# Performance work log

Measured on AMD Instinct MI355X. Metric: run time of the kernel, lower is better.

Reference implementation:

```python
import jax, jax.numpy as jnp
import numpy as np
from jax import lax

B, QL, N_IN, H = 64, 2048, 256, 64


def setup_inputs() -> dict:
    key = jax.random.key(0)
    ks = jax.random.split(key, 8)
    s = 1.0 / np.sqrt(H)  # PyTorch LSTMCell init scale
    return {
        "h_concat": jax.random.normal(ks[0], (B, QL, N_IN), dtype=jnp.float32),
        "w21": jax.random.normal(ks[1], (N_IN, 1), dtype=jnp.float32),
        "w22": jax.random.normal(ks[2], (H, 1), dtype=jnp.float32),
        "bias2": jax.random.normal(ks[3], (1,), dtype=jnp.float32),
        "W_ih": jax.random.uniform(ks[4], (4 * H, N_IN + 1), dtype=jnp.float32, minval=-s, maxval=s),
        "W_hh": jax.random.uniform(ks[5], (4 * H, H), dtype=jnp.float32, minval=-s, maxval=s),
        "b_ih": jax.random.uniform(ks[6], (4 * H,), dtype=jnp.float32, minval=-s, maxval=s),
        "b_hh": jax.random.uniform(ks[7], (4 * H,), dtype=jnp.float32, minval=-s, maxval=s),
    }


def reference(h_concat, w21, w22, bias2, W_ih, W_hh, b_ih, b_hh):
    Bsz, T, n_in = h_concat.shape
    nh = W_hh.shape[1]

    def step(carry, x):
        h, c = carry  # [B,H] each; x: [B,n_in]
        # sigmoid gate: pz_t = sigmoid(x @ w21 + h @ w22 + bias2) -> [B,1]
        pz = jax.nn.sigmoid(x @ w21 + h @ w22 + bias2)
        hz = jnp.concatenate([x, pz], axis=1)  # [B, n_in+1]
        # LSTMCell (PyTorch gate order: i, f, g, o)
        gates = hz @ W_ih.T + b_ih + h @ W_hh.T + b_hh  # [B,4H]
        i, f, g, o = jnp.split(gates, 4, axis=1)
        c_new = jax.nn.sigmoid(f) * c + jax.nn.sigmoid(i) * jnp.tanh(g)
        h_new = jax.nn.sigmoid(o) * jnp.tanh(c_new)
        return (h_new, c_new), pz[:, 0]

    h0 = jnp.zeros((Bsz, nh), dtype=h_concat.dtype)
    c0 = jnp.zeros((Bsz, nh), dtype=h_concat.dtype)
    xs = jnp.swapaxes(h_concat, 0, 1)  # [T,B,n_in]
    _, Z = lax.scan(step, (h0, c0), xs)  # Z: [T,B]
    return jnp.swapaxes(Z, 0, 1)  # [B,T]
```

## Files before the change

kernel.cpp:

```cpp
#include <hip/hip_runtime.h>

#define TT 2048
#define BB 64

typedef _Float16 v2h __attribute__((ext_vector_type(2)));
typedef _Float16 v4h __attribute__((ext_vector_type(4)));
typedef float v4f __attribute__((ext_vector_type(4)));

__device__ __forceinline__ float frcp(float x) { return __builtin_amdgcn_rcpf(x); }
__device__ __forceinline__ float fsig(float x) { return frcp(1.f + __expf(-x)); }
__device__ __forceinline__ float ftan(float x) { return 1.f - 2.f * frcp(1.f + __expf(2.f * x)); }

#if __has_builtin(__builtin_amdgcn_fdot2)
#define FDOT2(a, b, c) __builtin_amdgcn_fdot2((a), (b), (c), false)
#else
#define FDOT2(a, b, c) ((c) + (float)(a).x * (float)(b).x + (float)(a).y * (float)(b).y)
#endif

#define DPPADD(x, ctrl)                                                        \
  (x) += __builtin_bit_cast(float, __builtin_amdgcn_update_dpp(                \
             0, __builtin_bit_cast(int, (x)), (ctrl), 0xf, 0xf, true))

__device__ __forceinline__ float wave_sum64(float x) {
  DPPADD(x, 0x111);
  DPPADD(x, 0x112);
  DPPADD(x, 0x114);
  DPPADD(x, 0x118);
  DPPADD(x, 0x142);
  DPPADD(x, 0x143);
  return __builtin_bit_cast(
      float, __builtin_amdgcn_readlane(__builtin_bit_cast(int, x), 63));
}

__global__ __launch_bounds__(256) void gates_gemm_mfma(
    const float* __restrict__ X, const float* __restrict__ W,
    const float* __restrict__ bih, const float* __restrict__ bhh,
    float* __restrict__ G, int t0, int Tc) {
  __shared__ __align__(16) _Float16 Xs[64][40];
  __shared__ __align__(16) _Float16 Ws[128][40];
  const int tid = threadIdx.x;
  const int m0 = blockIdx.x * 64;
  const int n0 = blockIdx.y * 128;
  const int bb = m0 / Tc;
  const int tt0 = m0 - bb * Tc;
  const int w = tid >> 6, l = tid & 63;
  const int lr = l & 15, lk = l >> 4;

  const int srow = tid >> 2, skq = (tid & 3) * 8;
  const int wri = tid >> 1, wkh = (tid & 1) * 16;
  const float* xrow = X + (size_t)(bb * TT + t0 + tt0 + srow) * 256 + skq;
  const float* wrow = W + (size_t)(n0 + wri) * 257 + wkh;

  float bsum[8];
#pragma unroll
  for (int nf = 0; nf < 8; ++nf)
    bsum[nf] = bih[n0 + nf * 16 + lr] + bhh[n0 + nf * 16 + lr];

  v4f acc[8];
#pragma unroll
  for (int nf = 0; nf < 8; ++nf) acc[nf] = (v4f){0.f, 0.f, 0.f, 0.f};

  for (int k0 = 0; k0 < 256; k0 += 32) {
    float xa[8], wa[16];
#pragma unroll
    for (int u = 0; u < 8; ++u) xa[u] = xrow[k0 + u];
#pragma unroll
    for (int u = 0; u < 16; ++u) wa[u] = wrow[k0 + u];
    if (k0 != 0) __syncthreads();
    {
      uint xw[4];
#pragma unroll
      for (int u = 0; u < 4; ++u) {
        v2h p; p.x = (_Float16)xa[2*u]; p.y = (_Float16)xa[2*u+1];
        xw[u] = __builtin_bit_cast(uint, p);
      }
      *reinterpret_cast<uint4*>(&Xs[srow][skq]) =
          make_uint4(xw[0], xw[1], xw[2], xw[3]);
      uint ww[8];
#pragma unroll
      for (int u = 0; u < 8; ++u) {
        v2h p; p.x = (_Float16)wa[2*u]; p.y = (_Float16)wa[2*u+1];
        ww[u] = __builtin_bit_cast(uint, p);
      }
      *reinterpret_cast<uint4*>(&Ws[wri][wkh]) =
          make_uint4(ww[0], ww[1], ww[2], ww[3]);
      *reinterpret_cast<uint4*>(&Ws[wri][wkh + 8]) =
          make_uint4(ww[4], ww[5], ww[6], ww[7]);
    }
    __syncthreads();
    const v4h a0 = *reinterpret_cast<const v4h*>(&Xs[w * 16 + lr][lk * 4]);
    const v4h a1 = *reinterpret_cast<const v4h*>(&Xs[w * 16 + lr][16 + lk * 4]);
#pragma unroll
    for (int nf = 0; nf < 8; ++nf) {
      const v4h b0 = *reinterpret_cast<const v4h*>(&Ws[nf * 16 + lr][lk * 4]);
      const v4h b1 = *reinterpret_cast<const v4h*>(&Ws[nf * 16 + lr][16 + lk * 4]);
      acc[nf] = __builtin_amdgcn_mfma_f32_16x16x16f16(a0, b0, acc[nf], 0, 0, 0);
      acc[nf] = __builtin_amdgcn_mfma_f32_16x16x16f16(a1, b1, acc[nf], 0, 0, 0);
    }
  }
  const int grow = m0 + w * 16 + lk * 4;
#pragma unroll
  for (int nf = 0; nf < 8; ++nf) {
#pragma unroll
    for (int j = 0; j < 4; ++j) {
      G[(size_t)(grow + j) * 256 + n0 + nf * 16 + lr] = acc[nf][j] + bsum[nf];
    }
  }
}

__global__ __launch_bounds__(256) void pz_kernel(const float* __restrict__ X,
                                                 const float* __restrict__ w21,
                                                 const float* __restrict__ bias2,
                                                 float* __restrict__ P,
                                                 int t0, int Tc) {
  const int r = blockIdx.x * 4 + (threadIdx.x >> 6);
  const int lane = threadIdx.x & 63;
  const int bb = r / Tc;
  const int tt = r - bb * Tc;
  const float4 xv = *reinterpret_cast<const float4*>(
      &X[((size_t)(bb * TT + t0 + tt)) * 256 + lane * 4]);
  const float4 wv = *reinterpret_cast<const float4*>(&w21[lane * 4]);
  float s = xv.x*wv.x + xv.y*wv.y + xv.z*wv.z + xv.w*wv.w;
#pragma unroll
  for (int o = 32; o; o >>= 1) s += __shfl_xor(s, o);
  if (lane == 0) P[r] = s + bias2[0];
}

__global__ __launch_bounds__(64, 1) void lstm_seq7(
    const float* __restrict__ G, const float* __restrict__ P,
    const float* __restrict__ Wih, const float* __restrict__ Whh,
    const float* __restrict__ w22, float* __restrict__ Z,
    float* __restrict__ hq, float* __restrict__ cq, int t0, int Tc) {
  const int l = threadIdx.x;
  const int b = blockIdx.x;
  __shared__ __align__(16) _Float16 hsm[64];

  v2h wh[4][32];
#pragma unroll
  for (int q = 0; q < 4; ++q) {
#pragma unroll
    for (int j = 0; j < 16; ++j) {
      float4 v = *reinterpret_cast<const float4*>(&Whh[(size_t)(q*64 + l)*64 + 4*j]);
      v2h pA, pB;
      pA.x = (_Float16)v.x; pA.y = (_Float16)v.y;
      pB.x = (_Float16)v.z; pB.y = (_Float16)v.w;
      wh[q][2*j] = pA; wh[q][2*j+1] = pB;
    }
  }
  float wihL[4];
#pragma unroll
  for (int q = 0; q < 4; ++q) wihL[q] = Wih[(size_t)(q*64 + l)*257 + 256];
  const float w22r = w22[l];

  float h = 0.f, c = 0.f;
  if (t0 != 0) { h = hq[b * 64 + l]; c = cq[b * 64 + l]; }
  hsm[l] = (_Float16)h;
  __builtin_amdgcn_wave_barrier();

  const float* Gb = G + (size_t)b * Tc * 256 + l;
  const float* Pb = P + (size_t)b * Tc;
  float* Zb = Z + (size_t)b * TT + t0;

  float gr[4][4], pr[4];
#pragma unroll
  for (int u = 0; u < 4; ++u) {
    const float* Gt = Gb + (size_t)u * 256;
#pragma unroll
    for (int q = 0; q < 4; ++q) gr[u][q] = Gt[q * 64];
    pr[u] = Pb[u];
  }

  for (int tt = 0; tt < Tc; tt += 4) {
    float zs[4];
#pragma unroll
    for (int uu = 0; uu < 4; ++uu) {
      const int step = tt + uu;
      const float gx0 = gr[uu][0], gx1 = gr[uu][1];
      const float gx2 = gr[uu][2], gx3 = gr[uu][3];
      const float p0 = pr[uu];
      int pf = step + 4; if (pf > Tc - 1) pf = Tc - 1;
      {
        const float* Gt = Gb + (size_t)pf * 256;
#pragma unroll
        for (int q = 0; q < 4; ++q) gr[uu][q] = Gt[q * 64];
        pr[uu] = Pb[pf];
      }

      const float tot = wave_sum64(h * w22r);
      const float pz = fsig(tot + p0);

      float d0a=0.f,d0b=0.f,d1a=0.f,d1b=0.f,d2a=0.f,d2b=0.f,d3a=0.f,d3b=0.f;
      const uint4* hp = reinterpret_cast<const uint4*>(hsm);
#pragma unroll
      for (int jj = 0; jj < 8; ++jj) {
        const uint4 uq = hp[jj];
        const v2h ha = __builtin_bit_cast(v2h, uq.x);
        const v2h hb = __builtin_bit_cast(v2h, uq.y);
        const v2h hc = __builtin_bit_cast(v2h, uq.z);
        const v2h hd = __builtin_bit_cast(v2h, uq.w);
        d0a = FDOT2(ha, wh[0][4*jj+0], d0a); d0b = FDOT2(hb, wh[0][4*jj+1], d0b);
        d0a = FDOT2(hc, wh[0][4*jj+2], d0a); d0b = FDOT2(hd, wh[0][4*jj+3], d0b);
        d1a = FDOT2(ha, wh[1][4*jj+0], d1a); d1b = FDOT2(hb, wh[1][4*jj+1], d1b);
        d1a = FDOT2(hc, wh[1][4*jj+2], d1a); d1b = FDOT2(hd, wh[1][4*jj+3], d1b);
        d2a = FDOT2(ha, wh[2][4*jj+0], d2a); d2b = FDOT2(hb, wh[2][4*jj+1], d2b);
        d2a = FDOT2(hc, wh[2][4*jj+2], d2a); d2b = FDOT2(hd, wh[2][4*jj+3], d2b);
        d3a = FDOT2(ha, wh[3][4*jj+0], d3a); d3b = FDOT2(hb, wh[3][4*jj+1], d3b);
        d3a = FDOT2(hc, wh[3][4*jj+2], d3a); d3b = FDOT2(hd, wh[3][4*jj+3], d3b);
      }
      const float pre0 = gx0 + pz * wihL[0] + (d0a + d0b);
      const float pre1 = gx1 + pz * wihL[1] + (d1a + d1b);
      const float pre2 = gx2 + pz * wihL[2] + (d2a + d2b);
      const float pre3 = gx3 + pz * wihL[3] + (d3a + d3b);

      const float ai = fsig(pre0);
      const float af = fsig(pre1);
      const float ag = ftan(pre2);
      const float ao = fsig(pre3);
      c = af * c + ai * ag;
      h = ao * ftan(c);

      __builtin_amdgcn_wave_barrier();
      hsm[l] = (_Float16)h;
      __builtin_amdgcn_wave_barrier();
      zs[uu] = pz;
    }
    if (l == 0) {
      float4 zo; zo.x = zs[0]; zo.y = zs[1]; zo.z = zs[2]; zo.w = zs[3];
      *reinterpret_cast<float4*>(&Zb[tt]) = zo;
    }
  }
  hq[b * 64 + l] = h;
  cq[b * 64 + l] = c;
}

__global__ __launch_bounds__(256) void lstm_fallback(const float* __restrict__ X,
    const float* __restrict__ w21, const float* __restrict__ w22,
    const float* __restrict__ bias2, const float* __restrict__ Wih,
    const float* __restrict__ Whh, const float* __restrict__ bih,
    const float* __restrict__ bhh, float* __restrict__ Z) {
  const int b = blockIdx.x;
  const int g = threadIdx.x;
  const int lane = g & 63;
  __shared__ __align__(16) float h_s[64];
  __shared__ float act_s[256];
  __shared__ __align__(16) float x_s[256];
  __shared__ __align__(16) float w21_s[256];
  float wh[64];
#pragma unroll
  for (int j = 0; j < 64; j += 4) {
    float4 v = *reinterpret_cast<const float4*>(&Whh[(size_t)g*64 + j]);
    wh[j]=v.x; wh[j+1]=v.y; wh[j+2]=v.z; wh[j+3]=v.w;
  }
  const float wihL = Wih[(size_t)g*257 + 256];
  const float bias = bih[g] + bhh[g];
  const float b2 = bias2[0];
  const float w22r = w22[lane];
  w21_s[g] = w21[g];
  if (g < 64) h_s[g] = 0.f;
  float c = 0.f;
  __syncthreads();
  const float* Wr = Wih + (size_t)g * 257;
  for (int t = 0; t < TT; ++t) {
    x_s[g] = X[((size_t)b*TT + t)*256 + g];
    __syncthreads();
    float pv = h_s[lane] * w22r;
    {
      const float4 xq = *reinterpret_cast<const float4*>(&x_s[lane*4]);
      const float4 wq = *reinterpret_cast<const float4*>(&w21_s[lane*4]);
      pv += xq.x*wq.x + xq.y*wq.y + xq.z*wq.z + xq.w*wq.w;
    }
#pragma unroll
    for (int o = 32; o; o >>= 1) pv += __shfl_xor(pv, o);
    const float pz = fsig(pv + b2);
    float a0=0.f, a1=0.f, a2=0.f, a3=0.f;
#pragma unroll
    for (int j = 0; j < 64; j += 4) {
      float4 hv = *reinterpret_cast<const float4*>(&h_s[j]);
      a0 += hv.x*wh[j]; a1 += hv.y*wh[j+1]; a2 += hv.z*wh[j+2]; a3 += hv.w*wh[j+3];
    }
    float xd0=0.f, xd1=0.f, xd2=0.f, xd3=0.f;
    for (int k = 0; k < 256; k += 4) {
      const float4 xq = *reinterpret_cast<const float4*>(&x_s[k]);
      xd0 += xq.x*Wr[k]; xd1 += xq.y*Wr[k+1]; xd2 += xq.z*Wr[k+2]; xd3 += xq.w*Wr[k+3];
    }
    const float pre = bias + pz*wihL + ((a0+a1)+(a2+a3)) + ((xd0+xd1)+(xd2+xd3));
    act_s[g] = ((g >> 6) == 2) ? ftan(pre) : fsig(pre);
    if (g == 0) Z[(size_t)b*TT + t] = pz;
    __syncthreads();
    if (g < 64) {
      const float iv = act_s[g], fv = act_s[64+g], gv = act_s[128+g], ov = act_s[192+g];
      c = fv*c + iv*gv;
      h_s[g] = ov * ftan(c);
    }
    __syncthreads();
  }
}

extern "C" void kernel_launch(void* const* d_in, const int* in_sizes, int n_in,
                              void* d_out, int out_size, void* d_ws, size_t ws_size,
                              hipStream_t stream) {
  const float* X     = (const float*)d_in[0];
  const float* w21   = (const float*)d_in[1];
  const float* w22   = (const float*)d_in[2];
  const float* bias2 = (const float*)d_in[3];
  const float* Wih   = (const float*)d_in[4];
  const float* Whh   = (const float*)d_in[5];
  const float* bih   = (const float*)d_in[6];
  const float* bhh   = (const float*)d_in[7];
  float* Z = (float*)d_out;

  int Tc = 0;
  for (int cand = 2048; cand >= 64; cand >>= 1) {
    size_t need = (size_t)cand * (64*256*4 + 64*4) + 2*64*64*4;
    if (ws_size >= need) { Tc = cand; break; }
  }
  if (Tc == 0) {
    lstm_fallback<<<dim3(64), dim3(256), 0, stream>>>(X, w21, w22, bias2, Wih, Whh, bih, bhh, Z);
    return;
  }
  float* Gbuf = (float*)d_ws;
  float* Pbuf = Gbuf + (size_t)64 * Tc * 256;
  float* hq   = Pbuf + (size_t)64 * Tc;
  float* cq   = hq + 64 * 64;
  for (int t0 = 0; t0 < 2048; t0 += Tc) {
    gates_gemm_mfma<<<dim3(Tc, 2), dim3(256), 0, stream>>>(X, Wih, bih, bhh,
                                                           Gbuf, t0, Tc);
    pz_kernel<<<dim3(16 * Tc), dim3(256), 0, stream>>>(X, w21, bias2, Pbuf, t0, Tc);
    lstm_seq7<<<dim3(BB), dim3(64), 0, stream>>>(
        Gbuf, Pbuf, Wih, Whh, w22, Z, hq, cq, t0, Tc);
  }
}
```

Baseline: 1.049 ms.

## Fuse pz projection into gates GEMM and widen recurrent dot-product accumulators

The separate pz_kernel is removed. The x·w21 projection is now computed inside the gates GEMM from the fp32 X values already loaded there, with w21 staged in shared memory and a 4-lane shuffle reduction. This saves one kernel launch and a second full read of X per chunk. The recurrent FDOT2 loop also uses four independent accumulators per gate instead of two, shortening the dependent chain on the serial LSTM critical path at the cost of more registers.

Measured after the change: 1.117 ms. 6.5% more time.

```diff
diff --git a/kernel.cpp b/kernel.cpp
--- a/kernel.cpp
+++ b/kernel.cpp
@@ -35,9 +35,11 @@
 __global__ __launch_bounds__(256) void gates_gemm_mfma(
     const float* __restrict__ X, const float* __restrict__ W,
     const float* __restrict__ bih, const float* __restrict__ bhh,
-    float* __restrict__ G, int t0, int Tc) {
+    const float* __restrict__ w21, const float* __restrict__ bias2,
+    float* __restrict__ G, float* __restrict__ P, int t0, int Tc) {
   __shared__ __align__(16) _Float16 Xs[64][40];
   __shared__ __align__(16) _Float16 Ws[128][40];
+  __shared__ float w21s[256];
   const int tid = threadIdx.x;
   const int m0 = blockIdx.x * 64;
   const int n0 = blockIdx.y * 128;
@@ -45,12 +47,15 @@
   const int tt0 = m0 - bb * Tc;
   const int w = tid >> 6, l = tid & 63;
   const int lr = l & 15, lk = l >> 4;
+  const bool do_pz = (blockIdx.y == 0);
 
   const int srow = tid >> 2, skq = (tid & 3) * 8;
   const int wri = tid >> 1, wkh = (tid & 1) * 16;
   const float* xrow = X + (size_t)(bb * TT + t0 + tt0 + srow) * 256 + skq;
   const float* wrow = W + (size_t)(n0 + wri) * 257 + wkh;
 
+  w21s[tid] = w21[tid];
+
   float bsum[8];
 #pragma unroll
   for (int nf = 0; nf < 8; ++nf)
@@ -59,6 +64,7 @@
   v4f acc[8];
 #pragma unroll
   for (int nf = 0; nf < 8; ++nf) acc[nf] = (v4f){0.f, 0.f, 0.f, 0.f};
+  float psum = 0.f;
 
   for (int k0 = 0; k0 < 256; k0 += 32) {
     float xa[8], wa[16];
@@ -88,6 +94,10 @@
           make_uint4(ww[4], ww[5], ww[6], ww[7]);
     }
     __syncthreads();
+    if (do_pz) {
+#pragma unroll
+      for (int u = 0; u < 8; ++u) psum += xa[u] * w21s[k0 + skq + u];
+    }
     const v4h a0 = *reinterpret_cast<const v4h*>(&Xs[w * 16 + lr][lk * 4]);
     const v4h a1 = *reinterpret_cast<const v4h*>(&Xs[w * 16 + lr][16 + lk * 4]);
 #pragma unroll
@@ -98,6 +108,11 @@
       acc[nf] = __builtin_amdgcn_mfma_f32_16x16x16f16(a1, b1, acc[nf], 0, 0, 0);
     }
   }
+  if (do_pz) {
+    psum += __shfl_xor(psum, 1);
+    psum += __shfl_xor(psum, 2);
+    if ((tid & 3) == 0) P[m0 + srow] = psum + bias2[0];
+  }
   const int grow = m0 + w * 16 + lk * 4;
 #pragma unroll
   for (int nf = 0; nf < 8; ++nf) {
@@ -108,25 +123,7 @@
   }
 }
 
-__global__ __launch_bounds__(256) void pz_kernel(const float* __restrict__ X,
-                                                 const float* __restrict__ w21,
-                                                 const float* __restrict__ bias2,
-                                                 float* __restrict__ P,
-                                                 int t0, int Tc) {
-  const int r = blockIdx.x * 4 + (threadIdx.x >> 6);
-  const int lane = threadIdx.x & 63;
-  const int bb = r / Tc;
-  const int tt = r - bb * Tc;
-  const float4 xv = *reinterpret_cast<const float4*>(
-      &X[((size_t)(bb * TT + t0 + tt)) * 256 + lane * 4]);
-  const float4 wv = *reinterpret_cast<const float4*>(&w21[lane * 4]);
-  float s = xv.x*wv.x + xv.y*wv.y + xv.z*wv.z + xv.w*wv.w;
-#pragma unroll
-  for (int o = 32; o; o >>= 1) s += __shfl_xor(s, o);
-  if (lane == 0) P[r] = s + bias2[0];
-}
-
-__global__ __launch_bounds__(64, 1) void lstm_seq7(
+__global__ __launch_bounds__(64, 1) void lstm_seq8(
     const float* __restrict__ G, const float* __restrict__ P,
     const float* __restrict__ Wih, const float* __restrict__ Whh,
     const float* __restrict__ w22, float* __restrict__ Z,
@@ -189,7 +186,8 @@
       const float tot = wave_sum64(h * w22r);
       const float pz = fsig(tot + p0);
 
-      float d0a=0.f,d0b=0.f,d1a=0.f,d1b=0.f,d2a=0.f,d2b=0.f,d3a=0.f,d3b=0.f;
+      float d0[4] = {0.f,0.f,0.f,0.f}, d1[4] = {0.f,0.f,0.f,0.f};
+      float d2[4] = {0.f,0.f,0.f,0.f}, d3[4] = {0.f,0.f,0.f,0.f};
       const uint4* hp = reinterpret_cast<const uint4*>(hsm);
 #pragma unroll
       for (int jj = 0; jj < 8; ++jj) {
@@ -198,19 +196,19 @@
         const v2h hb = __builtin_bit_cast(v2h, uq.y);
         const v2h hc = __builtin_bit_cast(v2h, uq.z);
         const v2h hd = __builtin_bit_cast(v2h, uq.w);
-        d0a = FDOT2(ha, wh[0][4*jj+0], d0a); d0b = FDOT2(hb, wh[0][4*jj+1], d0b);
-        d0a = FDOT2(hc, wh[0][4*jj+2], d0a); d0b = FDOT2(hd, wh[0][4*jj+3], d0b);
-        d1a = FDOT2(ha, wh[1][4*jj+0], d1a); d1b = FDOT2(hb, wh[1][4*jj+1], d1b);
-        d1a = FDOT2(hc, wh[1][4*jj+2], d1a); d1b = FDOT2(hd, wh[1][4*jj+3], d1b);
-        d2a = FDOT2(ha, wh[2][4*jj+0], d2a); d2b = FDOT2(hb, wh[2][4*jj+1], d2b);
-        d2a = FDOT2(hc, wh[2][4*jj+2], d2a); d2b = FDOT2(hd, wh[2][4*jj+3], d2b);
-        d3a = FDOT2(ha, wh[3][4*jj+0], d3a); d3b = FDOT2(hb, wh[3][4*jj+1], d3b);
-        d3a = FDOT2(hc, wh[3][4*jj+2], d3a); d3b = FDOT2(hd, wh[3][4*jj+3], d3b);
+        d0[0] = FDOT2(ha, wh[0][4*jj+0], d0[0]); d0[1] = FDOT2(hb, wh[0][4*jj+1], d0[1]);
+        d0[2] = FDOT2(hc, wh[0][4*jj+2], d0[2]); d0[3] = FDOT2(hd, wh[0][4*jj+3], d0[3]);
+        d1[0] = FDOT2(ha, wh[1][4*jj+0], d1[0]); d1[1] = FDOT2(hb, wh[1][4*jj+1], d1[1]);
+        d1[2] = FDOT2(hc, wh[1][4*jj+2], d1[2]); d1[3] = FDOT2(hd, wh[1][4*jj+3], d1[3]);
+        d2[0] = FDOT2(ha, wh[2][4*jj+0], d2[0]); d2[1] = FDOT2(hb, wh[2][4*jj+1], d2[1]);
+        d2[2] = FDOT2(hc, wh[2][4*jj+2], d2[2]); d2[3] = FDOT2(hd, wh[2][4*jj+3], d2[3]);
+        d3[0] = FDOT2(ha, wh[3][4*jj+0], d3[0]); d3[1] = FDOT2(hb, wh[3][4*jj+1], d3[1]);
+        d3[2] = FDOT2(hc, wh[3][4*jj+2], d3[2]); d3[3] = FDOT2(hd, wh[3][4*jj+3], d3[3]);
       }
-      const float pre0 = gx0 + pz * wihL[0] + (d0a + d0b);
-      const float pre1 = gx1 + pz * wihL[1] + (d1a + d1b);
-      const float pre2 = gx2 + pz * wihL[2] + (d2a + d2b);
-      const float pre3 = gx3 + pz * wihL[3] + (d3a + d3b);
+      const float pre0 = gx0 + pz * wihL[0] + ((d0[0]+d0[1]) + (d0[2]+d0[3]));
+      const float pre1 = gx1 + pz * wihL[1] + ((d1[0]+d1[1]) + (d1[2]+d1[3]));
+      const float pre2 = gx2 + pz * wihL[2] + ((d2[0]+d2[1]) + (d2[2]+d2[3]));
+      const float pre3 = gx3 + pz * wihL[3] + ((d3[0]+d3[1]) + (d3[2]+d3[3]));
 
       const float ai = fsig(pre0);
       const float af = fsig(pre1);
@@ -323,10 +321,9 @@
   float* hq   = Pbuf + (size_t)64 * Tc;
   float* cq   = hq + 64 * 64;
   for (int t0 = 0; t0 < 2048; t0 += Tc) {
-    gates_gemm_mfma<<<dim3(Tc, 2), dim3(256), 0, stream>>>(X, Wih, bih, bhh,
-                                                           Gbuf, t0, Tc);
-    pz_kernel<<<dim3(16 * Tc), dim3(256), 0, stream>>>(X, w21, bias2, Pbuf, t0, Tc);
-    lstm_seq7<<<dim3(BB), dim3(64), 0, stream>>>(
+    gates_gemm_mfma<<<dim3(Tc, 2), dim3(256), 0, stream>>>(
+        X, Wih, bih, bhh, w21, bias2, Gbuf, Pbuf, t0, Tc);
+    lstm_seq8<<<dim3(BB), dim3(64), 0, stream>>>(
         Gbuf, Pbuf, Wih, Whh, w22, Z, hq, cq, t0, Tc);
   }
 }
```
